# Optimization experiments

Measured on AMD Instinct MI355X. Metric: run time of the kernel, lower is better.

The kernel has to match this reference:

```python
import jax, jax.numpy as jnp
import numpy as np

N = 50000
E = 600000
IN = 128
HID = 128
OUT = 64
EPS = 1e-5


def layernorm(x, g, b):
    mu = jnp.mean(x, axis=-1, keepdims=True)
    var = jnp.mean(jnp.square(x - mu), axis=-1, keepdims=True)
    return (x - mu) * jax.lax.rsqrt(var + EPS) * g + b


def film_layer(x, W, Fm, g, b, src, dst):
    # x: [N, d_in]; W: [d_out, d_in]; Fm: [2*d_out, d_in]
    m = x @ W.T                       # [N, d_out]
    fw = x @ Fm.T                     # [N, 2*d_out]
    d_out = W.shape[0]
    gamma, beta = fw[:, :d_out], fw[:, d_out:]
    msg = jax.nn.relu(gamma * m + beta)           # [N, d_out]
    h = jax.ops.segment_sum(msg[src], dst, num_segments=N)  # scatter-sum over edges
    return layernorm(h, g, b)  # dropout is identity in eval mode


def setup_inputs() -> dict:
    key = jax.random.key(0)
    ks = jax.random.split(key, 12)
    s = lambda fan_in: 1.0 / np.sqrt(fan_in)
    return {
        "features": jax.random.normal(ks[0], (N, IN), dtype=jnp.float32),
        "src": jax.random.randint(ks[1], (E,), 0, N, dtype=jnp.int32),
        "dst": jax.random.randint(ks[2], (E,), 0, N, dtype=jnp.int32),
        "W1": jax.random.uniform(ks[3], (HID, IN), jnp.float32, -s(IN), s(IN)),
        "F1": jax.random.uniform(ks[4], (2 * HID, IN), jnp.float32, -s(IN), s(IN)),
        "g1": jnp.ones((HID,), jnp.float32),
        "b1": jnp.zeros((HID,), jnp.float32),
        "W2": jax.random.uniform(ks[5], (HID, HID), jnp.float32, -s(HID), s(HID)),
        "F2": jax.random.uniform(ks[6], (2 * HID, HID), jnp.float32, -s(HID), s(HID)),
        "g2": jnp.ones((HID,), jnp.float32),
        "b2": jnp.zeros((HID,), jnp.float32),
        "Wp": jax.random.uniform(ks[7], (OUT, HID), jnp.float32, -s(HID), s(HID)),
        "bp": jax.random.uniform(ks[8], (OUT,), jnp.float32, -s(HID), s(HID)),
    }


def reference(features, src, dst, W1, F1, g1, b1, W2, F2, g2, b2, Wp, bp):
    h = film_layer(features, W1, F1, g1, b1, src, dst)
    h = film_layer(h, W2, F2, g2, b2, src, dst)
    return jax.nn.sigmoid(h @ Wp.T + bp)  # [N, OUT]
```

## Files before the change

### kernel.cpp

```cpp
#include <hip/hip_runtime.h>
#include <hip/hip_bf16.h>
#include <math.h>

#define IN_D 128
#define HID_D 128
#define OUT_D 64
#define CAP 64

typedef __attribute__((ext_vector_type(8))) short bf16x8;
typedef __attribute__((ext_vector_type(4))) float f32x4;

__device__ __forceinline__ unsigned short f2bf(float f) {
    unsigned u = __float_as_uint(f);
    u += 0x7fffu + ((u >> 16) & 1u);
    return (unsigned short)(u >> 16);
}
__device__ __forceinline__ float bf2f(unsigned short h) {
    return __uint_as_float(((unsigned)h) << 16);
}

__global__ __launch_bounds__(256) void k_fill_prep(
        const int* __restrict__ src_idx, const int* __restrict__ dst_idx,
        int* __restrict__ cnt, unsigned short* __restrict__ elist, int E,
        const float* __restrict__ W1, const float* __restrict__ F1,
        const float* __restrict__ W2, const float* __restrict__ F2,
        const float* __restrict__ Wp,
        const float* __restrict__ X, unsigned short* __restrict__ fx, int nfv,
        unsigned short* __restrict__ wc1, unsigned short* __restrict__ wc2,
        unsigned short* __restrict__ wpb) {
    int e = blockIdx.x * 256 + threadIdx.x;
    if (e < E) {
        int d = dst_idx[e];
        int pos = atomicAdd(&cnt[d], 1);
        elist[(size_t)d * CAP + pos] = (unsigned short)src_idx[e];
    }
    if (e < nfv) {
        const float4* xp = (const float4*)X + (size_t)e * 4;
        float4 v0 = xp[0], v1 = xp[1], v2 = xp[2], v3 = xp[3];
        uint4 o0, o1;
        o0.x = (unsigned)f2bf(v0.x) | ((unsigned)f2bf(v0.y) << 16);
        o0.y = (unsigned)f2bf(v0.z) | ((unsigned)f2bf(v0.w) << 16);
        o0.z = (unsigned)f2bf(v1.x) | ((unsigned)f2bf(v1.y) << 16);
        o0.w = (unsigned)f2bf(v1.z) | ((unsigned)f2bf(v1.w) << 16);
        o1.x = (unsigned)f2bf(v2.x) | ((unsigned)f2bf(v2.y) << 16);
        o1.y = (unsigned)f2bf(v2.z) | ((unsigned)f2bf(v2.w) << 16);
        o1.z = (unsigned)f2bf(v3.x) | ((unsigned)f2bf(v3.y) << 16);
        o1.w = (unsigned)f2bf(v3.z) | ((unsigned)f2bf(v3.w) << 16);
        ((uint4*)fx)[(size_t)e * 2]     = o0;
        ((uint4*)fx)[(size_t)e * 2 + 1] = o1;
    }
    const int NW = HID_D * IN_D;
    const int NC = 3 * NW;
    const int NP = OUT_D * HID_D;
    int i = e;
    if (i < NC) {
        wc1[i] = f2bf(i < NW ? W1[i] : F1[i - NW]);
    } else if (i < 2 * NC) {
        int j = i - NC;
        wc2[j] = f2bf(j < NW ? W2[j] : F2[j - NW]);
    } else if (i < 2 * NC + NP) {
        int j = i - 2 * NC;
        wpb[j] = f2bf(Wp[j]);
    }
}

__global__ __launch_bounds__(256, 2) void k_msg(const unsigned short* __restrict__ X,
                                                const unsigned short* __restrict__ Wc,
                                                unsigned short* __restrict__ Msg,
                                                int n, int nchunks) {
    const int wave = threadIdx.x >> 6;
    const int lane = threadIdx.x & 63;
    const int lr = lane & 15;
    const int quad = lane >> 4;
    const int t0 = wave * 2;
    const int tidx[6] = {t0, t0 + 1, t0 + 8, t0 + 9, t0 + 16, t0 + 17};

    bf16x8 b[6][4];
    #pragma unroll
    for (int u = 0; u < 6; u++)
        #pragma unroll
        for (int s = 0; s < 4; s++)
            b[u][s] = *(const bf16x8*)(Wc + (size_t)(16 * tidx[u] + lr) * IN_D + quad * 8 + 32 * s);

    for (int c = blockIdx.x; c < nchunks; c += gridDim.x) {
        const int row0 = c << 4;

        int r = row0 + lr;
        if (r > n - 1) r = n - 1;
        const unsigned short* xp = X + (size_t)r * IN_D + quad * 8;
        bf16x8 a[4];
        #pragma unroll
        for (int s = 0; s < 4; s++) a[s] = *(const bf16x8*)(xp + 32 * s);

        f32x4 acc[6];
        #pragma unroll
        for (int u = 0; u < 6; u++) acc[u] = (f32x4){0.f, 0.f, 0.f, 0.f};

        #pragma unroll
        for (int s = 0; s < 4; s++)
            #pragma unroll
            for (int u = 0; u < 6; u++)
                acc[u] = __builtin_amdgcn_mfma_f32_16x16x32_bf16(a[s], b[u][s], acc[u], 0, 0, 0);

        #pragma unroll
        for (int u = 0; u < 2; u++) {
            #pragma unroll
            for (int rr = 0; rr < 4; rr++) {
                int row = row0 + quad * 4 + rr;
                if (row < n) {
                    float v = acc[2 + u][rr] * acc[u][rr] + acc[4 + u][rr];
                    v = v > 0.f ? v : 0.f;
                    Msg[(size_t)row * HID_D + 16 * (t0 + u) + lr] = f2bf(v);
                }
            }
        }
    }
}

__global__ __launch_bounds__(256) void k_agg_ln(const unsigned short* __restrict__ Msg,
                                                const unsigned short* __restrict__ elist,
                                                const int* __restrict__ cnt,
                                                const float* __restrict__ gamma,
                                                const float* __restrict__ beta,
                                                unsigned short* __restrict__ Hout, int n) {
    int node = blockIdx.x * 4 + (threadIdx.x >> 6);
    int lane = threadIdx.x & 63;
    int half = lane >> 5;
    int l = lane & 31;
    if (node >= n) return;
    const unsigned short* seg = elist + (size_t)node * CAP;
    int deg = cnt[node];
    int myidx = seg[lane];
    float a0 = 0.f, a1 = 0.f, a2 = 0.f, a3 = 0.f;

#define ACC4(v) { a0 += bf2f((unsigned short)((v).x & 0xffffu)); \
                  a1 += bf2f((unsigned short)((v).x >> 16));     \
                  a2 += bf2f((unsigned short)((v).y & 0xffffu)); \
                  a3 += bf2f((unsigned short)((v).y >> 16)); }

    int i = 0;
    for (; i + 4 <= deg; i += 4) {
        int iA = __shfl(myidx, i + half);
        int iB = __shfl(myidx, i + 2 + half);
        uint2 vA = *(const uint2*)(Msg + (size_t)iA * HID_D + l * 4);
        uint2 vB = *(const uint2*)(Msg + (size_t)iB * HID_D + l * 4);
        ACC4(vA);
        ACC4(vB);
    }
    for (; i + 2 <= deg; i += 2) {
        int iA = __shfl(myidx, i + half);
        uint2 vA = *(const uint2*)(Msg + (size_t)iA * HID_D + l * 4);
        ACC4(vA);
    }
    if (i < deg && half == 0) {
        int iA = __shfl(myidx, i);
        uint2 vA = *(const uint2*)(Msg + (size_t)iA * HID_D + l * 4);
        ACC4(vA);
    }
#undef ACC4

    a0 += __shfl_xor(a0, 32);
    a1 += __shfl_xor(a1, 32);
    a2 += __shfl_xor(a2, 32);
    a3 += __shfl_xor(a3, 32);

    float s = a0 + a1 + a2 + a3;
    float sq = a0 * a0 + a1 * a1 + a2 * a2 + a3 * a3;
    #pragma unroll
    for (int d = 16; d; d >>= 1) {
        s += __shfl_xor(s, d);
        sq += __shfl_xor(sq, d);
    }
    float mu = s * (1.f / 128.f);
    float var = sq * (1.f / 128.f) - mu * mu;
    float rs = rsqrtf(var + 1e-5f);
    float4 g4 = ((const float4*)gamma)[l];
    float4 b4 = ((const float4*)beta)[l];
    float y0 = (a0 - mu) * rs * g4.x + b4.x;
    float y1 = (a1 - mu) * rs * g4.y + b4.y;
    float y2 = (a2 - mu) * rs * g4.z + b4.z;
    float y3 = (a3 - mu) * rs * g4.w + b4.w;
    if (half == 0) {
        uint2 o;
        o.x = (unsigned)f2bf(y0) | ((unsigned)f2bf(y1) << 16);
        o.y = (unsigned)f2bf(y2) | ((unsigned)f2bf(y3) << 16);
        *(uint2*)(Hout + (size_t)node * HID_D + l * 4) = o;
    }
}

__global__ __launch_bounds__(256) void k_proj(const unsigned short* __restrict__ H,
                                              const unsigned short* __restrict__ Wpb,
                                              const float* __restrict__ bp,
                                              float* __restrict__ out, int n) {
    const int row0 = blockIdx.x << 6;
    const int wave = threadIdx.x >> 6;
    const int lane = threadIdx.x & 63;
    const int lr = lane & 15;
    const int quad = lane >> 4;

    f32x4 acc[4];
    #pragma unroll
    for (int rt = 0; rt < 4; rt++) acc[rt] = (f32x4){0.f, 0.f, 0.f, 0.f};

    #pragma unroll
    for (int s = 0; s < 4; s++) {
        bf16x8 bv = *(const bf16x8*)(Wpb + (size_t)(16 * wave + lr) * HID_D + quad * 8 + 32 * s);
        #pragma unroll
        for (int rt = 0; rt < 4; rt++) {
            int r = row0 + rt * 16 + lr;
            if (r > n - 1) r = n - 1;
            bf16x8 av = *(const bf16x8*)(H + (size_t)r * HID_D + quad * 8 + 32 * s);
            acc[rt] = __builtin_amdgcn_mfma_f32_16x16x32_bf16(av, bv, acc[rt], 0, 0, 0);
        }
    }
    float bias = bp[16 * wave + lr];
    #pragma unroll
    for (int rt = 0; rt < 4; rt++) {
        #pragma unroll
        for (int r = 0; r < 4; r++) {
            int row = row0 + rt * 16 + quad * 4 + r;
            if (row < n) {
                float z = acc[rt][r] + bias;
                out[(size_t)row * OUT_D + 16 * wave + lr] = 1.f / (1.f + __expf(-z));
            }
        }
    }
}

extern "C" void kernel_launch(void* const* d_in, const int* in_sizes, int n_in,
                              void* d_out, int out_size, void* d_ws, size_t ws_size,
                              hipStream_t stream) {
    const float* features = (const float*)d_in[0];
    const int* src = (const int*)d_in[1];
    const int* dst = (const int*)d_in[2];
    const float* W1 = (const float*)d_in[3];
    const float* F1 = (const float*)d_in[4];
    const float* g1 = (const float*)d_in[5];
    const float* b1 = (const float*)d_in[6];
    const float* W2 = (const float*)d_in[7];
    const float* F2 = (const float*)d_in[8];
    const float* g2 = (const float*)d_in[9];
    const float* b2 = (const float*)d_in[10];
    const float* Wp = (const float*)d_in[11];
    const float* bp = (const float*)d_in[12];

    const int N = in_sizes[0] / IN_D;
    const int E = in_sizes[1];
    float* out = (float*)d_out;

    char* p = (char*)d_ws;
    auto alloc = [&](size_t b) -> char* {
        char* r = p;
        p += (b + 255) & ~(size_t)255;
        return r;
    };
    unsigned short* buf0 = (unsigned short*)alloc((size_t)N * HID_D * 2);
    unsigned short* buf1 = (unsigned short*)alloc((size_t)N * HID_D * 2);
    unsigned short* fx   = (unsigned short*)alloc((size_t)N * IN_D * 2);
    unsigned short* wc1  = (unsigned short*)alloc((size_t)3 * HID_D * IN_D * 2);
    unsigned short* wc2  = (unsigned short*)alloc((size_t)3 * HID_D * HID_D * 2);
    unsigned short* wpb  = (unsigned short*)alloc((size_t)OUT_D * HID_D * 2);
    int* cnt    = (int*)alloc((size_t)N * 4);
    unsigned short* elist = (unsigned short*)alloc((size_t)N * CAP * 2);

    const int eb = (E + 255) / 256;
    const int mc = (N + 15) / 16;
    const int mg = 512;
    const int pb = (N + 63) / 64;
    const int ab = (N + 3) / 4;
    const int nfv = (N * IN_D) / 16;

    hipMemsetAsync(cnt, 0, (size_t)N * 4, stream);
    k_fill_prep<<<eb, 256, 0, stream>>>(src, dst, cnt, elist, E,
                                        W1, F1, W2, F2, Wp,
                                        features, fx, nfv, wc1, wc2, wpb);

    k_msg<<<mg, 256, 0, stream>>>(fx, wc1, buf1, N, mc);
    k_agg_ln<<<ab, 256, 0, stream>>>(buf1, elist, cnt, g1, b1, buf0, N);
    k_msg<<<mg, 256, 0, stream>>>(buf0, wc2, buf1, N, mc);
    k_agg_ln<<<ab, 256, 0, stream>>>(buf1, elist, cnt, g2, b2, buf0, N);
    k_proj<<<pb, 256, 0, stream>>>(buf0, wpb, bp, out, N);
}
```

Before: 233.5 us.

## Move edge-list fill into first message kernel and zero counts in prep

```diff
diff --git a/kernel.cpp b/kernel.cpp
--- a/kernel.cpp
+++ b/kernel.cpp
@@ -19,21 +19,16 @@
     return __uint_as_float(((unsigned)h) << 16);
 }
 
-__global__ __launch_bounds__(256) void k_fill_prep(
-        const int* __restrict__ src_idx, const int* __restrict__ dst_idx,
-        int* __restrict__ cnt, unsigned short* __restrict__ elist, int E,
+__global__ __launch_bounds__(256) void k_prep(
         const float* __restrict__ W1, const float* __restrict__ F1,
         const float* __restrict__ W2, const float* __restrict__ F2,
         const float* __restrict__ Wp,
         const float* __restrict__ X, unsigned short* __restrict__ fx, int nfv,
         unsigned short* __restrict__ wc1, unsigned short* __restrict__ wc2,
-        unsigned short* __restrict__ wpb) {
+        unsigned short* __restrict__ wpb,
+        int* __restrict__ cnt, int n) {
     int e = blockIdx.x * 256 + threadIdx.x;
-    if (e < E) {
-        int d = dst_idx[e];
-        int pos = atomicAdd(&cnt[d], 1);
-        elist[(size_t)d * CAP + pos] = (unsigned short)src_idx[e];
-    }
+    if (e < n) cnt[e] = 0;
     if (e < nfv) {
         const float4* xp = (const float4*)X + (size_t)e * 4;
         float4 v0 = xp[0], v1 = xp[1], v2 = xp[2], v3 = xp[3];
@@ -64,10 +59,27 @@
     }
 }
 
+template <bool FILL>
 __global__ __launch_bounds__(256, 2) void k_msg(const unsigned short* __restrict__ X,
                                                 const unsigned short* __restrict__ Wc,
                                                 unsigned short* __restrict__ Msg,
-                                                int n, int nchunks) {
+                                                int n, int nchunks,
+                                                const int* __restrict__ src_idx,
+                                                const int* __restrict__ dst_idx,
+                                                int* __restrict__ cnt,
+                                                unsigned short* __restrict__ elist,
+                                                int E, int epb) {
+    if (FILL) {
+        int e0 = blockIdx.x * epb;
+        int e1 = e0 + epb;
+        if (e1 > E) e1 = E;
+        for (int e = e0 + threadIdx.x; e < e1; e += 256) {
+            int d = dst_idx[e];
+            int pos = atomicAdd(&cnt[d], 1);
+            elist[(size_t)d * CAP + pos] = (unsigned short)src_idx[e];
+        }
+    }
+
     const int wave = threadIdx.x >> 6;
     const int lane = threadIdx.x & 63;
     const int lr = lane & 15;
@@ -263,21 +275,22 @@
     int* cnt    = (int*)alloc((size_t)N * 4);
     unsigned short* elist = (unsigned short*)alloc((size_t)N * CAP * 2);
 
-    const int eb = (E + 255) / 256;
     const int mc = (N + 15) / 16;
     const int mg = 512;
     const int pb = (N + 63) / 64;
     const int ab = (N + 3) / 4;
     const int nfv = (N * IN_D) / 16;
-
-    hipMemsetAsync(cnt, 0, (size_t)N * 4, stream);
-    k_fill_prep<<<eb, 256, 0, stream>>>(src, dst, cnt, elist, E,
-                                        W1, F1, W2, F2, Wp,
-                                        features, fx, nfv, wc1, wc2, wpb);
-
-    k_msg<<<mg, 256, 0, stream>>>(fx, wc1, buf1, N, mc);
+    const int gb = (nfv + 255) / 256;
+    const int epb = (E + mg - 1) / mg;
+
+    k_prep<<<gb, 256, 0, stream>>>(W1, F1, W2, F2, Wp,
+                                   features, fx, nfv, wc1, wc2, wpb, cnt, N);
+
+    k_msg<true><<<mg, 256, 0, stream>>>(fx, wc1, buf1, N, mc,
+                                        src, dst, cnt, elist, E, epb);
     k_agg_ln<<<ab, 256, 0, stream>>>(buf1, elist, cnt, g1, b1, buf0, N);
-    k_msg<<<mg, 256, 0, stream>>>(buf0, wc2, buf1, N, mc);
+    k_msg<false><<<mg, 256, 0, stream>>>(buf0, wc2, buf1, N, mc,
+                                         nullptr, nullptr, nullptr, nullptr, 0, 0);
     k_agg_ln<<<ab, 256, 0, stream>>>(buf1, elist, cnt, g2, b2, buf0, N);
     k_proj<<<pb, 256, 0, stream>>>(buf0, wpb, bp, out, N);
 }
```

Result: no change. 234.1 us (+0.3%).
